# Kernel tuning notes

Hardware: AMD Instinct MI355X
Metric: run time of the kernel (lower is better)

The kernel has to match this reference:

```python
import jax, jax.numpy as jnp
import numpy as np

C_IN = 256
C_INT = C_IN // 2  # inter_channels


def _conv1x1(x, w, b):
    # x: [B, Cin, H, W], w: [Cout, Cin], b: [Cout]
    return jnp.einsum('bchw,oc->bohw', x, w) + b[None, :, None, None]


def setup_inputs() -> dict:
    key = jax.random.key(0)
    ks = jax.random.split(key, 9)
    B, H, W = 8, 64, 64
    s_in = 1.0 / np.sqrt(C_IN)
    s_int = 1.0 / np.sqrt(C_INT)
    return {
        'x': jax.random.normal(ks[0], (B, C_IN, H, W), dtype=jnp.float32),
        'g_w': jax.random.normal(ks[1], (C_INT, C_IN), dtype=jnp.float32) * s_in,
        'g_b': jax.random.normal(ks[2], (C_INT,), dtype=jnp.float32) * s_in,
        'theta_w': jax.random.normal(ks[3], (C_INT, C_IN), dtype=jnp.float32) * s_in,
        'theta_b': jax.random.normal(ks[4], (C_INT,), dtype=jnp.float32) * s_in,
        'phi_w': jax.random.normal(ks[5], (C_INT, C_IN), dtype=jnp.float32) * s_in,
        'phi_b': jax.random.normal(ks[6], (C_INT,), dtype=jnp.float32) * s_in,
        'W_w': jax.random.normal(ks[7], (C_IN, C_INT), dtype=jnp.float32) * s_int,
        'W_b': jax.random.normal(ks[8], (C_IN,), dtype=jnp.float32) * s_int,
    }


def reference(x, g_w, g_b, theta_w, theta_b, phi_w, phi_b, W_w, W_b):
    B, C, H, W = x.shape
    N = H * W
    g_x = _conv1x1(x, g_w, g_b).reshape(B, C_INT, N)        # [B, Ci, N]
    theta_x = _conv1x1(x, theta_w, theta_b).reshape(B, C_INT, N)
    phi_x = _conv1x1(x, phi_w, phi_b).reshape(B, C_INT, N)
    # f[b, i, j] = theta[:, i] . phi[:, j]  (no scaling, per original)
    f = jnp.einsum('bci,bcj->bij', theta_x, phi_x)          # [B, N, N]
    f_div_C = jax.nn.softmax(f, axis=-1)
    y = jnp.einsum('bij,bcj->bci', f_div_C, g_x)            # [B, Ci, N]
    y = y.reshape(B, C_INT, H, W)
    y = _conv1x1(y, W_w, W_b)                               # [B, C, H, W]
    return x + y
```

## Files before the change

kernel.cpp:

```cpp
#include <hip/hip_runtime.h>

typedef _Float16 f16;
typedef _Float16 f16x2 __attribute__((ext_vector_type(2)));
typedef _Float16 f16x4 __attribute__((ext_vector_type(4)));
typedef _Float16 f16x8 __attribute__((ext_vector_type(8)));
typedef float f32x4 __attribute__((ext_vector_type(4)));
typedef float f32x16 __attribute__((ext_vector_type(16)));

#define MFMA16(a, b, c) __builtin_amdgcn_mfma_f32_16x16x32_f16(a, b, c, 0, 0, 0)
#define MFMA32(a, b, c) __builtin_amdgcn_mfma_f32_32x32x16_f16(a, b, c, 0, 0, 0)

__device__ __forceinline__ int swzr(int row) { return ((row & 7) << 4) ^ ((row & 8) << 2); }

__global__ __launch_bounds__(256) void wcvt_k(
    const float* __restrict__ tw, const float* __restrict__ pw,
    const float* __restrict__ gw, const float* __restrict__ ww,
    f16* __restrict__ Wall, f16* __restrict__ Wepi) {
  int i = blockIdx.x * 256 + threadIdx.x;
  if (i < 384 * 256) {
    int c = i >> 8, cp = i & 255;
    float v = (c < 128) ? tw[c * 256 + cp]
            : (c < 256) ? pw[(c - 128) * 256 + cp]
                        : gw[(c - 256) * 256 + cp];
    Wall[i] = (f16)v;
  }
  int j = i - 384 * 256;
  if (j >= 0 && j < 256 * 128) Wepi[j] = (f16)ww[j];
}

__global__ __launch_bounds__(256) void xpose_k(const float* __restrict__ x,
                                               f16* __restrict__ xT) {
  __shared__ f16 t[64 * 65];
  int bx = blockIdx.x;
  int b = bx >> 8, rem = bx & 255;
  int c0 = (rem >> 6) * 64, n0 = (rem & 63) * 64;
  const float* xb = x + ((size_t)b * 256 + c0) * 4096 + n0;
#pragma unroll
  for (int rep = 0; rep < 16; ++rep) {
    int idx = rep * 256 + threadIdx.x;
    int i = idx >> 6, j = idx & 63;
    t[j * 65 + i] = (f16)xb[(size_t)i * 4096 + j];
  }
  __syncthreads();
  f16* o = xT + ((size_t)b * 4096 + n0) * 256 + c0;
#pragma unroll
  for (int rep = 0; rep < 16; ++rep) {
    int idx = rep * 256 + threadIdx.x;
    int j = idx >> 6, i = idx & 63;
    o[(size_t)j * 256 + i] = t[j * 65 + i];
  }
}

__global__ __launch_bounds__(256) void proj_k(
    const f16* __restrict__ xT, const f16* __restrict__ Wall,
    const float* __restrict__ tb, const float* __restrict__ pb,
    const float* __restrict__ gb, f16* __restrict__ Q, f16* __restrict__ K,
    f16* __restrict__ Vt) {
  __shared__ f16 vs[128 * 65];
  int b = blockIdx.x >> 6, nt = blockIdx.x & 63;
  int nbase = nt * 64;
  int w = threadIdx.x >> 6, lane = threadIdx.x & 63;
  int lr = lane & 15, lhi = lane >> 4;
  int nrow = nbase + w * 16 + lr;
  const f16x8* xr = (const f16x8*)(xT + ((size_t)b * 4096 + nrow) * 256);
  f16x8 a[8];
#pragma unroll
  for (int ks = 0; ks < 8; ++ks) a[ks] = xr[ks * 4 + lhi];
  f32x4 acc[24];
#pragma unroll
  for (int ct = 0; ct < 24; ++ct) {
    acc[ct] = {0.f, 0.f, 0.f, 0.f};
    const f16x8* wr = (const f16x8*)(Wall + (size_t)(ct * 16 + lr) * 256);
#pragma unroll
    for (int ks = 0; ks < 8; ++ks) acc[ct] = MFMA16(a[ks], wr[ks * 4 + lhi], acc[ct]);
  }
  int nloc = w * 16 + lhi * 4;
#pragma unroll
  for (int ct = 0; ct < 24; ++ct) {
    int c = ct * 16 + lr;
    float bias = (c < 128) ? tb[c] : (c < 256) ? pb[c - 128] : gb[c - 256];
#pragma unroll
    for (int r = 0; r < 4; ++r) {
      float v = acc[ct][r] + bias;
      int n = nbase + nloc + r;
      if (c < 128)
        Q[((size_t)b * 4096 + n) * 128 + c] = (f16)v;
      else if (c < 256)
        K[((size_t)b * 4096 + n) * 128 + (c - 128)] = (f16)v;
      else
        vs[(c - 256) * 65 + nloc + r] = (f16)v;
    }
  }
  __syncthreads();
  f16* vo = Vt + (size_t)b * 128 * 4096 + nbase;
  for (int rep = 0; rep < 32; ++rep) {
    int idx = rep * 256 + threadIdx.x;
    int c = idx >> 6, j = idx & 63;
    vo[(size_t)c * 4096 + j] = vs[c * 65 + j];
  }
}

__global__ __launch_bounds__(256, 2) void attn_k(const f16* __restrict__ Q,
                                                 const f16* __restrict__ K,
                                                 const f16* __restrict__ Vt,
                                                 f16* __restrict__ Yp01,
                                                 f16* __restrict__ Yp23,
                                                 float2* __restrict__ ml) {
  __shared__ f16 Ks[64 * 128];
  __shared__ f16 Vs[128 * 64];
  const float L = 1.44269504f;
  int swzid = ((blockIdx.x & 7) << 7) | ((int)blockIdx.x >> 3);
  int b = swzid >> 7, rem = swzid & 127;
  int qt = rem >> 2, s = rem & 3;
  int qbase = qt * 128;
  int kvbase = s << 10;
  int tid = threadIdx.x;
  int w = tid >> 6, lane = tid & 63;
  int col = lane & 31, hi = lane >> 5;

  const f16* Qr = Q + ((size_t)b * 4096 + qbase + w * 32 + col) * 128;
  f16x8 bq[8];
#pragma unroll
  for (int ks = 0; ks < 8; ++ks) bq[ks] = *(const f16x8*)(Qr + ks * 16 + hi * 8);

  f32x16 yacc[4];
#pragma unroll
  for (int dt = 0; dt < 4; ++dt)
#pragma unroll
    for (int r = 0; r < 16; ++r) yacc[dt][r] = 0.f;
  float lv[16];
#pragma unroll
  for (int r = 0; r < 16; ++r) lv[r] = 0.f;
  float m = -1e30f, nmL = 1e30f;

  const f16* Kbase = K + (size_t)b * 4096 * 128;
  const f16* Vbase = Vt + (size_t)b * 128 * 4096;

  int krow = tid >> 4, kcolb = (tid & 15) * 16;
  int vrow = tid >> 1, h2 = tid & 1;
  int sv = swzr(vrow);
  int vblo[4];
#pragma unroll
  for (int u = 0; u < 4; ++u) vblo[u] = h2 * 64 + (u & 2) * 16 + (u & 1) * 8;

  {
    const f16* Kt = Kbase + (size_t)kvbase * 128;
    f16x8 kr[4], vr[4];
#pragma unroll
    for (int r = 0; r < 4; ++r) kr[r] = *(const f16x8*)(Kt + (r * 256 + tid) * 8);
#pragma unroll
    for (int u = 0; u < 4; ++u)
      vr[u] = *(const f16x8*)(Vbase + (size_t)vrow * 4096 + kvbase + h2 * 32 + u * 8);
#pragma unroll
    for (int r = 0; r < 4; ++r) {
      int row = r * 16 + krow;
      *(f16x8*)((char*)Ks + row * 256 + (kcolb ^ swzr(row))) = kr[r];
    }
#pragma unroll
    for (int u = 0; u < 4; ++u) {
      f16x4 lo = {vr[u][0], vr[u][1], vr[u][2], vr[u][3]};
      f16x4 hi4 = {vr[u][4], vr[u][5], vr[u][6], vr[u][7]};
      *(f16x4*)((char*)Vs + vrow * 128 + (vblo[u] ^ sv)) = lo;
      *(f16x4*)((char*)Vs + vrow * 128 + ((vblo[u] + 16) ^ sv)) = hi4;
    }
  }

  for (int t = 0; t < 16; ++t) {
    f16x8 kr[4], vr[4];
    bool pf = (t + 1 < 16);
    if (pf) {
      int kv0 = kvbase + (t + 1) * 64;
      const f16* Kt = Kbase + (size_t)kv0 * 128;
#pragma unroll
      for (int r = 0; r < 4; ++r) kr[r] = *(const f16x8*)(Kt + (r * 256 + tid) * 8);
#pragma unroll
      for (int u = 0; u < 4; ++u)
        vr[u] = *(const f16x8*)(Vbase + (size_t)vrow * 4096 + kv0 + h2 * 32 + u * 8);
    }
    __syncthreads();

    f32x16 s2[2];
    __builtin_amdgcn_s_setprio(1);
#pragma unroll
    for (int t2 = 0; t2 < 2; ++t2) {
#pragma unroll
      for (int r = 0; r < 16; ++r) s2[t2][r] = 0.f;
      int row = t2 * 32 + col;
      const char* kb = (const char*)Ks + row * 256;
      int sk = swzr(row);
#pragma unroll
      for (int ks = 0; ks < 8; ++ks) {
        f16x8 ak = *(const f16x8*)(kb + ((ks * 32 + hi * 16) ^ sk));
        s2[t2] = MFMA32(ak, bq[ks], s2[t2]);
      }
    }
    __builtin_amdgcn_s_setprio(0);

    float v[16];
#pragma unroll
    for (int r = 0; r < 16; ++r) v[r] = fmaxf(s2[0][r], s2[1][r]);
    float t0 = fmaxf(fmaxf(v[0], v[1]), v[2]);
    float t1 = fmaxf(fmaxf(v[3], v[4]), v[5]);
    float t2 = fmaxf(fmaxf(v[6], v[7]), v[8]);
    float t3 = fmaxf(fmaxf(v[9], v[10]), v[11]);
    float t4 = fmaxf(fmaxf(v[12], v[13]), v[14]);
    float u0 = fmaxf(fmaxf(t0, t1), t2);
    float u1 = fmaxf(fmaxf(t3, t4), v[15]);
    float pm = fmaxf(u0, u1);
    pm = fmaxf(pm, __shfl_xor(pm, 32));
    if (pm > m + 8.f) {
      float sc = __expf(m - pm);
      m = pm;
      nmL = -m * L;
#pragma unroll
      for (int r = 0; r < 16; ++r) lv[r] *= sc;
#pragma unroll
      for (int dt = 0; dt < 4; ++dt)
#pragma unroll
        for (int r = 0; r < 16; ++r) yacc[dt][r] *= sc;
    }
#pragma unroll
    for (int t2i = 0; t2i < 2; ++t2i)
#pragma unroll
      for (int r = 0; r < 16; ++r) s2[t2i][r] = exp2f(fmaf(s2[t2i][r], L, nmL));
#pragma unroll
    for (int r = 0; r < 16; ++r) lv[r] += s2[0][r] + s2[1][r];

    f16x8 pfr[4];
#pragma unroll
    for (int t2i = 0; t2i < 2; ++t2i)
#pragma unroll
      for (int k1 = 0; k1 < 2; ++k1) {
        f16x8 f;
#pragma unroll
        for (int c = 0; c < 8; ++c) f[c] = (f16)s2[t2i][8 * k1 + c];
        pfr[t2i * 2 + k1] = f;
      }

    __builtin_amdgcn_s_setprio(1);
#pragma unroll
    for (int kstep = 0; kstep < 4; ++kstep) {
#pragma unroll
      for (int dt = 0; dt < 4; ++dt) {
        int row = dt * 32 + col;
        f16x8 av = *(const f16x8*)((const char*)Vs + row * 128 +
                                   ((kstep * 32 + hi * 16) ^ swzr(row)));
        yacc[dt] = MFMA32(av, pfr[kstep], yacc[dt]);
      }
    }
    __builtin_amdgcn_s_setprio(0);

    __syncthreads();
    if (pf) {
#pragma unroll
      for (int r = 0; r < 4; ++r) {
        int row = r * 16 + krow;
        *(f16x8*)((char*)Ks + row * 256 + (kcolb ^ swzr(row))) = kr[r];
      }
#pragma unroll
      for (int u = 0; u < 4; ++u) {
        f16x4 lo = {vr[u][0], vr[u][1], vr[u][2], vr[u][3]};
        f16x4 hi4 = {vr[u][4], vr[u][5], vr[u][6], vr[u][7]};
        *(f16x4*)((char*)Vs + vrow * 128 + (vblo[u] ^ sv)) = lo;
        *(f16x4*)((char*)Vs + vrow * 128 + ((vblo[u] + 16) ^ sv)) = hi4;
      }
    }
  }

  float l8[8], l4[4];
#pragma unroll
  for (int i = 0; i < 8; ++i) l8[i] = lv[i] + lv[i + 8];
#pragma unroll
  for (int i = 0; i < 4; ++i) l4[i] = l8[i] + l8[i + 4];
  float l = (l4[0] + l4[1]) + (l4[2] + l4[3]);
  l += __shfl_xor(l, 32);

  int rowG = b * 4096 + qbase + w * 32 + col;
  f16* yo = (s < 2 ? Yp01 : Yp23) + ((size_t)(s & 1) * 32768 + rowG) * 128;
  float inv = 1.0f / l;
#pragma unroll
  for (int dt = 0; dt < 4; ++dt)
#pragma unroll
    for (int a = 0; a < 4; ++a) {
      f16x4 ov = {(f16)(yacc[dt][4 * a] * inv), (f16)(yacc[dt][4 * a + 1] * inv),
                  (f16)(yacc[dt][4 * a + 2] * inv), (f16)(yacc[dt][4 * a + 3] * inv)};
      *(f16x4*)(yo + dt * 32 + a * 8 + hi * 4) = ov;
    }
  if (hi == 0) ml[s * 32768 + rowG] = make_float2(m, l);
}

__global__ __launch_bounds__(256) void epi_k(const f16* __restrict__ Yp01,
                                             const f16* __restrict__ Yp23,
                                             const float2* __restrict__ ml,
                                             const f16* __restrict__ Wepi,
                                             const float* __restrict__ Wb,
                                             const float* __restrict__ x,
                                             float* __restrict__ out) {
  int b = blockIdx.x >> 6, nt = blockIdx.x & 63;
  int nbase = nt * 64;
  int w = threadIdx.x >> 6, lane = threadIdx.x & 63;
  int lr = lane & 15, lhi = lane >> 4;
  const f16* yb0 = Yp01;
  const f16* yb1 = Yp01 + (size_t)32768 * 128;
  const f16* yb2 = Yp23;
  const f16* yb3 = Yp23 + (size_t)32768 * 128;
  f16x8 by[4][4];
#pragma unroll
  for (int n4 = 0; n4 < 4; ++n4) {
    int row = b * 4096 + nbase + n4 * 16 + lr;
    float2 m0 = ml[row], m1 = ml[32768 + row], m2 = ml[65536 + row], m3 = ml[98304 + row];
    float mm = fmaxf(fmaxf(m0.x, m1.x), fmaxf(m2.x, m3.x));
    float w0 = m0.y * __expf(m0.x - mm), w1 = m1.y * __expf(m1.x - mm);
    float w2 = m2.y * __expf(m2.x - mm), w3 = m3.y * __expf(m3.x - mm);
    float inv = 1.f / (w0 + w1 + w2 + w3);
    w0 *= inv; w1 *= inv; w2 *= inv; w3 *= inv;
    size_t rb = (size_t)row * 128;
#pragma unroll
    for (int ks = 0; ks < 4; ++ks) {
      int eo = ks * 32 + lhi * 8;
      f16x8 a0 = *(const f16x8*)(yb0 + rb + eo);
      f16x8 a1 = *(const f16x8*)(yb1 + rb + eo);
      f16x8 a2 = *(const f16x8*)(yb2 + rb + eo);
      f16x8 a3 = *(const f16x8*)(yb3 + rb + eo);
      f16x8 o;
#pragma unroll
      for (int e = 0; e < 8; ++e)
        o[e] = (f16)(w0 * (float)a0[e] + w1 * (float)a1[e] + w2 * (float)a2[e] +
                     w3 * (float)a3[e]);
      by[n4][ks] = o;
    }
  }
#pragma unroll
  for (int ot = 0; ot < 4; ++ot) {
    int o0 = w * 64 + ot * 16;
    const f16x8* wr = (const f16x8*)(Wepi + (size_t)(o0 + lr) * 128);
    f16x8 a[4];
#pragma unroll
    for (int ks = 0; ks < 4; ++ks) a[ks] = wr[ks * 4 + lhi];
#pragma unroll
    for (int n4 = 0; n4 < 4; ++n4) {
      f32x4 acc = {0.f, 0.f, 0.f, 0.f};
#pragma unroll
      for (int ks = 0; ks < 4; ++ks) acc = MFMA16(a[ks], by[n4][ks], acc);
#pragma unroll
      for (int r = 0; r < 4; ++r) {
        int o = o0 + lhi * 4 + r;
        int n = nbase + n4 * 16 + lr;
        size_t idx = ((size_t)b * 256 + o) * 4096 + n;
        out[idx] = x[idx] + Wb[o] + acc[r];
      }
    }
  }
}

extern "C" void kernel_launch(void* const* d_in, const int* in_sizes, int n_in,
                              void* d_out, int out_size, void* d_ws, size_t ws_size,
                              hipStream_t stream) {
  const float* x       = (const float*)d_in[0];
  const float* g_w     = (const float*)d_in[1];
  const float* g_b     = (const float*)d_in[2];
  const float* theta_w = (const float*)d_in[3];
  const float* theta_b = (const float*)d_in[4];
  const float* phi_w   = (const float*)d_in[5];
  const float* phi_b   = (const float*)d_in[6];
  const float* W_w     = (const float*)d_in[7];
  const float* W_b     = (const float*)d_in[8];
  float* out = (float*)d_out;

  f16* xT   = (f16*)d_ws;
  f16* Q    = xT + (size_t)8 * 4096 * 256;
  f16* Kk   = Q + (size_t)8 * 4096 * 128;
  f16* Vt   = Kk + (size_t)8 * 4096 * 128;
  f16* Wall = Vt + (size_t)8 * 4096 * 128;
  f16* Wepi = Wall + 384 * 256;
  float2* ml = (float2*)(Wepi + 256 * 128);
  f16* Yp23 = (f16*)(ml + 4 * 32768);
  f16* Yp01 = xT;

  wcvt_k<<<512, 256, 0, stream>>>(theta_w, phi_w, g_w, W_w, Wall, Wepi);
  xpose_k<<<2048, 256, 0, stream>>>(x, xT);
  proj_k<<<512, 256, 0, stream>>>(xT, Wall, theta_b, phi_b, g_b, Q, Kk, Vt);
  attn_k<<<1024, 256, 0, stream>>>(Q, Kk, Vt, Yp01, Yp23, ml);
  epi_k<<<512, 256, 0, stream>>>(Yp01, Yp23, ml, Wepi, W_b, x, out);
}
```

Before: 196.7 us.

## Fuse transpose into projection, double-buffer attention LDS, halve KV split count

Removes the separate transpose kernel: the projection kernel now loads fp32 x directly, converts it to fp16 and transposes it through shared memory. The attention kernel now splits KV into 2 halves instead of 4, launching 512 blocks with 32 tiles each. It double-buffers the K/V shared tiles to drop one barrier per iteration and packs the V stores as 8-wide writes. The epilogue merges only 2 partials, which cuts the partial-output traffic. In exchange there are fewer attention blocks to spread across the CUs, and the larger LDS footprint may lower occupancy.

```diff
diff --git a/kernel.cpp b/kernel.cpp
--- a/kernel.cpp
+++ b/kernel.cpp
@@ -1,7 +1,6 @@
 #include <hip/hip_runtime.h>
 
 typedef _Float16 f16;
-typedef _Float16 f16x2 __attribute__((ext_vector_type(2)));
 typedef _Float16 f16x4 __attribute__((ext_vector_type(4)));
 typedef _Float16 f16x8 __attribute__((ext_vector_type(8)));
 typedef float f32x4 __attribute__((ext_vector_type(4)));
@@ -28,44 +27,40 @@
   if (j >= 0 && j < 256 * 128) Wepi[j] = (f16)ww[j];
 }
 
-__global__ __launch_bounds__(256) void xpose_k(const float* __restrict__ x,
-                                               f16* __restrict__ xT) {
-  __shared__ f16 t[64 * 65];
-  int bx = blockIdx.x;
-  int b = bx >> 8, rem = bx & 255;
-  int c0 = (rem >> 6) * 64, n0 = (rem & 63) * 64;
-  const float* xb = x + ((size_t)b * 256 + c0) * 4096 + n0;
-#pragma unroll
-  for (int rep = 0; rep < 16; ++rep) {
-    int idx = rep * 256 + threadIdx.x;
-    int i = idx >> 6, j = idx & 63;
-    t[j * 65 + i] = (f16)xb[(size_t)i * 4096 + j];
-  }
-  __syncthreads();
-  f16* o = xT + ((size_t)b * 4096 + n0) * 256 + c0;
-#pragma unroll
-  for (int rep = 0; rep < 16; ++rep) {
-    int idx = rep * 256 + threadIdx.x;
-    int j = idx >> 6, i = idx & 63;
-    o[(size_t)j * 256 + i] = t[j * 65 + i];
-  }
-}
-
 __global__ __launch_bounds__(256) void proj_k(
-    const f16* __restrict__ xT, const f16* __restrict__ Wall,
+    const float* __restrict__ x, const f16* __restrict__ Wall,
     const float* __restrict__ tb, const float* __restrict__ pb,
     const float* __restrict__ gb, f16* __restrict__ Q, f16* __restrict__ K,
     f16* __restrict__ Vt) {
+  __shared__ f16 xs[64 * 264];
   __shared__ f16 vs[128 * 65];
   int b = blockIdx.x >> 6, nt = blockIdx.x & 63;
   int nbase = nt * 64;
-  int w = threadIdx.x >> 6, lane = threadIdx.x & 63;
+  int tid = threadIdx.x;
+
+  int nq = tid & 15, kq0 = tid >> 4;
+#pragma unroll
+  for (int p = 0; p < 4; ++p) {
+    int kq = kq0 + 16 * p;
+    float4 ld[4];
+#pragma unroll
+    for (int j = 0; j < 4; ++j)
+      ld[j] = *(const float4*)(x + ((size_t)b * 256 + 4 * kq + j) * 4096 + nbase + 4 * nq);
+#pragma unroll
+    for (int e = 0; e < 4; ++e) {
+      f16x4 wv = {(f16)((&ld[0].x)[e]), (f16)((&ld[1].x)[e]), (f16)((&ld[2].x)[e]),
+                  (f16)((&ld[3].x)[e])};
+      *(f16x4*)(&xs[(4 * nq + e) * 264 + 4 * kq]) = wv;
+    }
+  }
+  __syncthreads();
+
+  int w = tid >> 6, lane = tid & 63;
   int lr = lane & 15, lhi = lane >> 4;
-  int nrow = nbase + w * 16 + lr;
-  const f16x8* xr = (const f16x8*)(xT + ((size_t)b * 4096 + nrow) * 256);
   f16x8 a[8];
 #pragma unroll
-  for (int ks = 0; ks < 8; ++ks) a[ks] = xr[ks * 4 + lhi];
+  for (int ks = 0; ks < 8; ++ks)
+    a[ks] = *(const f16x8*)(&xs[(w * 16 + lr) * 264 + ks * 32 + lhi * 8]);
   f32x4 acc[24];
 #pragma unroll
   for (int ct = 0; ct < 24; ++ct) {
@@ -103,17 +98,16 @@
 __global__ __launch_bounds__(256, 2) void attn_k(const f16* __restrict__ Q,
                                                  const f16* __restrict__ K,
                                                  const f16* __restrict__ Vt,
-                                                 f16* __restrict__ Yp01,
-                                                 f16* __restrict__ Yp23,
+                                                 f16* __restrict__ Yp,
                                                  float2* __restrict__ ml) {
-  __shared__ f16 Ks[64 * 128];
-  __shared__ f16 Vs[128 * 64];
+  __shared__ f16 Ks[2][64 * 128];
+  __shared__ f16 Vs[2][128 * 64];
   const float L = 1.44269504f;
-  int swzid = ((blockIdx.x & 7) << 7) | ((int)blockIdx.x >> 3);
-  int b = swzid >> 7, rem = swzid & 127;
-  int qt = rem >> 2, s = rem & 3;
+  int swzid = ((blockIdx.x & 7) << 6) | ((int)blockIdx.x >> 3);
+  int b = swzid >> 6, rem = swzid & 63;
+  int qt = rem >> 1, half = rem & 1;
   int qbase = qt * 128;
-  int kvbase = s << 10;
+  int kvbase = half << 11;
   int tid = threadIdx.x;
   int w = tid >> 6, lane = tid & 63;
   int col = lane & 31, hi = lane >> 5;
@@ -139,9 +133,6 @@
   int krow = tid >> 4, kcolb = (tid & 15) * 16;
   int vrow = tid >> 1, h2 = tid & 1;
   int sv = swzr(vrow);
-  int vblo[4];
-#pragma unroll
-  for (int u = 0; u < 4; ++u) vblo[u] = h2 * 64 + (u & 2) * 16 + (u & 1) * 8;
 
   {
     const f16* Kt = Kbase + (size_t)kvbase * 128;
@@ -154,20 +145,27 @@
 #pragma unroll
     for (int r = 0; r < 4; ++r) {
       int row = r * 16 + krow;
-      *(f16x8*)((char*)Ks + row * 256 + (kcolb ^ swzr(row))) = kr[r];
-    }
-#pragma unroll
-    for (int u = 0; u < 4; ++u) {
-      f16x4 lo = {vr[u][0], vr[u][1], vr[u][2], vr[u][3]};
-      f16x4 hi4 = {vr[u][4], vr[u][5], vr[u][6], vr[u][7]};
-      *(f16x4*)((char*)Vs + vrow * 128 + (vblo[u] ^ sv)) = lo;
-      *(f16x4*)((char*)Vs + vrow * 128 + ((vblo[u] + 16) ^ sv)) = hi4;
-    }
-  }
-
-  for (int t = 0; t < 16; ++t) {
+      *(f16x8*)((char*)Ks[0] + row * 256 + (kcolb ^ swzr(row))) = kr[r];
+    }
+    f16x8 c0, c1, c2, c3;
+#pragma unroll
+    for (int e = 0; e < 4; ++e) {
+      c0[e] = vr[0][e];     c0[4 + e] = vr[1][e];
+      c1[e] = vr[0][4 + e]; c1[4 + e] = vr[1][4 + e];
+      c2[e] = vr[2][e];     c2[4 + e] = vr[3][e];
+      c3[e] = vr[2][4 + e]; c3[4 + e] = vr[3][4 + e];
+    }
+    char* vb = (char*)Vs[0] + vrow * 128;
+    *(f16x8*)(vb + ((h2 * 64 + 0) ^ sv)) = c0;
+    *(f16x8*)(vb + ((h2 * 64 + 16) ^ sv)) = c1;
+    *(f16x8*)(vb + ((h2 * 64 + 32) ^ sv)) = c2;
+    *(f16x8*)(vb + ((h2 * 64 + 48) ^ sv)) = c3;
+  }
+
+  for (int t = 0; t < 32; ++t) {
+    int cur = t & 1, nxt = cur ^ 1;
     f16x8 kr[4], vr[4];
-    bool pf = (t + 1 < 16);
+    bool pf = (t + 1 < 32);
     if (pf) {
       int kv0 = kvbase + (t + 1) * 64;
       const f16* Kt = Kbase + (size_t)kv0 * 128;
@@ -186,7 +184,7 @@
 #pragma unroll
       for (int r = 0; r < 16; ++r) s2[t2][r] = 0.f;
       int row = t2 * 32 + col;
-      const char* kb = (const char*)Ks + row * 256;
+      const char* kb = (const char*)Ks[cur] + row * 256;
       int sk = swzr(row);
 #pragma unroll
       for (int ks = 0; ks < 8; ++ks) {
@@ -243,27 +241,32 @@
 #pragma unroll
       for (int dt = 0; dt < 4; ++dt) {
         int row = dt * 32 + col;
-        f16x8 av = *(const f16x8*)((const char*)Vs + row * 128 +
+        f16x8 av = *(const f16x8*)((const char*)Vs[cur] + row * 128 +
                                    ((kstep * 32 + hi * 16) ^ swzr(row)));
         yacc[dt] = MFMA32(av, pfr[kstep], yacc[dt]);
       }
     }
     __builtin_amdgcn_s_setprio(0);
 
-    __syncthreads();
     if (pf) {
 #pragma unroll
       for (int r = 0; r < 4; ++r) {
         int row = r * 16 + krow;
-        *(f16x8*)((char*)Ks + row * 256 + (kcolb ^ swzr(row))) = kr[r];
-      }
-#pragma unroll
-      for (int u = 0; u < 4; ++u) {
-        f16x4 lo = {vr[u][0], vr[u][1], vr[u][2], vr[u][3]};
-        f16x4 hi4 = {vr[u][4], vr[u][5], vr[u][6], vr[u][7]};
-        *(f16x4*)((char*)Vs + vrow * 128 + (vblo[u] ^ sv)) = lo;
-        *(f16x4*)((char*)Vs + vrow * 128 + ((vblo[u] + 16) ^ sv)) = hi4;
-      }
+        *(f16x8*)((char*)Ks[nxt] + row * 256 + (kcolb ^ swzr(row))) = kr[r];
+      }
+      f16x8 c0, c1, c2, c3;
+#pragma unroll
+      for (int e = 0; e < 4; ++e) {
+        c0[e] = vr[0][e];     c0[4 + e] = vr[1][e];
+        c1[e] = vr[0][4 + e]; c1[4 + e] = vr[1][4 + e];
+        c2[e] = vr[2][e];     c2[4 + e] = vr[3][e];
+        c3[e] = vr[2][4 + e]; c3[4 + e] = vr[3][4 + e];
+      }
+      char* vb = (char*)Vs[nxt] + vrow * 128;
+      *(f16x8*)(vb + ((h2 * 64 + 0) ^ sv)) = c0;
+      *(f16x8*)(vb + ((h2 * 64 + 16) ^ sv)) = c1;
+      *(f16x8*)(vb + ((h2 * 64 + 32) ^ sv)) = c2;
+      *(f16x8*)(vb + ((h2 * 64 + 48) ^ sv)) = c3;
     }
   }
 
@@ -276,7 +279,7 @@
   l += __shfl_xor(l, 32);
 
   int rowG = b * 4096 + qbase + w * 32 + col;
-  f16* yo = (s < 2 ? Yp01 : Yp23) + ((size_t)(s & 1) * 32768 + rowG) * 128;
+  f16* yo = Yp + ((size_t)half * 32768 + rowG) * 128;
   float inv = 1.0f / l;
 #pragma unroll
   for (int dt = 0; dt < 4; ++dt)
@@ -286,11 +289,10 @@
                   (f16)(yacc[dt][4 * a + 2] * inv), (f16)(yacc[dt][4 * a + 3] * inv)};
       *(f16x4*)(yo + dt * 32 + a * 8 + hi * 4) = ov;
     }
-  if (hi == 0) ml[s * 32768 + rowG] = make_float2(m, l);
-}
-
-__global__ __launch_bounds__(256) void epi_k(const f16* __restrict__ Yp01,
-                                             const f16* __restrict__ Yp23,
+  if (hi == 0) ml[half * 32768 + rowG] = make_float2(m, l);
+}
+
+__global__ __launch_bounds__(256) void epi_k(const f16* __restrict__ Yp,
                                              const float2* __restrict__ ml,
                                              const f16* __restrict__ Wepi,
                                              const float* __restrict__ Wb,
@@ -300,33 +302,26 @@
   int nbase = nt * 64;
   int w = threadIdx.x >> 6, lane = threadIdx.x & 63;
   int lr = lane & 15, lhi = lane >> 4;
-  const f16* yb0 = Yp01;
-  const f16* yb1 = Yp01 + (size_t)32768 * 128;
-  const f16* yb2 = Yp23;
-  const f16* yb3 = Yp23 + (size_t)32768 * 128;
+  const f16* yb1 = Yp + (size_t)32768 * 128;
   f16x8 by[4][4];
 #pragma unroll
   for (int n4 = 0; n4 < 4; ++n4) {
     int row = b * 4096 + nbase + n4 * 16 + lr;
-    float2 m0 = ml[row], m1 = ml[32768 + row], m2 = ml[65536 + row], m3 = ml[98304 + row];
-    float mm = fmaxf(fmaxf(m0.x, m1.x), fmaxf(m2.x, m3.x));
+    float2 m0 = ml[row], m1 = ml[32768 + row];
+    float mm = fmaxf(m0.x, m1.x);
     float w0 = m0.y * __expf(m0.x - mm), w1 = m1.y * __expf(m1.x - mm);
-    float w2 = m2.y * __expf(m2.x - mm), w3 = m3.y * __expf(m3.x - mm);
-    float inv = 1.f / (w0 + w1 + w2 + w3);
-    w0 *= inv; w1 *= inv; w2 *= inv; w3 *= inv;
+    float inv = 1.f / (w0 + w1);
+    w0 *= inv;
+    w1 *= inv;
     size_t rb = (size_t)row * 128;
 #pragma unroll
     for (int ks = 0; ks < 4; ++ks) {
       int eo = ks * 32 + lhi * 8;
-      f16x8 a0 = *(const f16x8*)(yb0 + rb + eo);
+      f16x8 a0 = *(const f16x8*)(Yp + rb + eo);
       f16x8 a1 = *(const f16x8*)(yb1 + rb + eo);
-      f16x8 a2 = *(const f16x8*)(yb2 + rb + eo);
-      f16x8 a3 = *(const f16x8*)(yb3 + rb + eo);
       f16x8 o;
 #pragma unroll
-      for (int e = 0; e < 8; ++e)
-        o[e] = (f16)(w0 * (float)a0[e] + w1 * (float)a1[e] + w2 * (float)a2[e] +
-                     w3 * (float)a3[e]);
+      for (int e = 0; e < 8; ++e) o[e] = (f16)(w0 * (float)a0[e] + w1 * (float)a1[e]);
       by[n4][ks] = o;
     }
   }
@@ -367,19 +362,16 @@
   const float* W_b     = (const float*)d_in[8];
   float* out = (float*)d_out;
 
-  f16* xT   = (f16*)d_ws;
-  f16* Q    = xT + (size_t)8 * 4096 * 256;
+  f16* Q    = (f16*)d_ws;
   f16* Kk   = Q + (size_t)8 * 4096 * 128;
   f16* Vt   = Kk + (size_t)8 * 4096 * 128;
   f16* Wall = Vt + (size_t)8 * 4096 * 128;
   f16* Wepi = Wall + 384 * 256;
   float2* ml = (float2*)(Wepi + 256 * 128);
-  f16* Yp23 = (f16*)(ml + 4 * 32768);
-  f16* Yp01 = xT;
+  f16* Yp   = (f16*)(ml + 2 * 32768);
 
   wcvt_k<<<512, 256, 0, stream>>>(theta_w, phi_w, g_w, W_w, Wall, Wepi);
-  xpose_k<<<2048, 256, 0, stream>>>(x, xT);
-  proj_k<<<512, 256, 0, stream>>>(xT, Wall, theta_b, phi_b, g_b, Q, Kk, Vt);
-  attn_k<<<1024, 256, 0, stream>>>(Q, Kk, Vt, Yp01, Yp23, ml);
-  epi_k<<<512, 256, 0, stream>>>(Yp01, Yp23, ml, Wepi, W_b, x, out);
-}
+  proj_k<<<512, 256, 0, stream>>>(x, Wall, theta_b, phi_b, g_b, Q, Kk, Vt);
+  attn_k<<<512, 256, 0, stream>>>(Q, Kk, Vt, Yp, ml);
+  epi_k<<<512, 256, 0, stream>>>(Yp, ml, Wepi, W_b, x, out);
+}
```

Result: faster. 186.9 us (-5.0%).
